# Kernel optimization log

Measured on AMD Instinct MI355X. Metric: run time of the kernel, lower is better.

## Reference

```python
import jax, jax.numpy as jnp
import numpy as np

S = 896.0          # image size in pixels
T = 28             # mask resolution
ALPHA, GAMMA = 0.25, 2.0
EPS = 1e-8
CAND_K = 10        # SimOTA candidate topk
CLS_W, L1_W, GIOU_W, MASK_W = 2.0, 5.0, 2.0, 5.0
CENTER_R = 0.05 * S  # center-region radius (approximates mmdet 2.5*stride)


def _areas(b):
    return jnp.clip(b[..., 2] - b[..., 0], 0) * jnp.clip(b[..., 3] - b[..., 1], 0)


def pairwise_iou_giou(a, b, eps=EPS):
    # a [n,4], b [m,4] xyxy -> (iou [n,m], giou [n,m])
    lt = jnp.maximum(a[:, None, :2], b[None, :, :2])
    rb = jnp.minimum(a[:, None, 2:], b[None, :, 2:])
    wh = jnp.clip(rb - lt, 0)
    inter = wh[..., 0] * wh[..., 1]
    union = _areas(a)[:, None] + _areas(b)[None, :] - inter
    iou = inter / (union + eps)
    elt = jnp.minimum(a[:, None, :2], b[None, :, :2])
    erb = jnp.maximum(a[:, None, 2:], b[None, :, 2:])
    ewh = jnp.clip(erb - elt, 0)
    enc = ewh[..., 0] * ewh[..., 1]
    return iou, iou - (enc - union) / (enc + eps)


def elementwise_giou(a, b, eps=EPS):
    # a,b [n,4] matched pairs -> giou [n] (the diag of generalized_box_iou)
    lt = jnp.maximum(a[:, :2], b[:, :2]); rb = jnp.minimum(a[:, 2:], b[:, 2:])
    wh = jnp.clip(rb - lt, 0); inter = wh[:, 0] * wh[:, 1]
    union = _areas(a) + _areas(b) - inter
    iou = inter / (union + eps)
    elt = jnp.minimum(a[:, :2], b[:, :2]); erb = jnp.maximum(a[:, 2:], b[:, 2:])
    ewh = jnp.clip(erb - elt, 0); enc = ewh[:, 0] * ewh[:, 1]
    return iou - (enc - union) / (enc + eps)


def crop_resize(img, box, scale, t=T):
    # img [C,H,W]; box [4] xyxy in image pixels; scale: pixels -> grid units.
    C, H, W = img.shape
    x1, y1, x2, y2 = box * scale
    xs = x1 + (x2 - x1) * (jnp.arange(t, dtype=img.dtype) + 0.5) / t - 0.5
    ys = y1 + (y2 - y1) * (jnp.arange(t, dtype=img.dtype) + 0.5) / t - 0.5
    X = jnp.broadcast_to(xs[None, :], (t, t))
    Y = jnp.broadcast_to(ys[:, None], (t, t))
    x0f = jnp.clip(jnp.floor(X), 0, W - 1); y0f = jnp.clip(jnp.floor(Y), 0, H - 1)
    wx = jnp.clip(X - x0f, 0, 1); wy = jnp.clip(Y - y0f, 0, 1)
    x0 = x0f.astype(jnp.int32); y0 = y0f.astype(jnp.int32)
    x1i = jnp.clip(x0 + 1, 0, W - 1); y1i = jnp.clip(y0 + 1, 0, H - 1)
    g = lambda yi, xi: img[:, yi, xi]  # [C,t,t]
    return (g(y0, x0) * (1 - wx) * (1 - wy) + g(y0, x1i) * wx * (1 - wy)
            + g(y1i, x0) * (1 - wx) * wy + g(y1i, x1i) * wx * wy)


def match_image(logits, boxes, gt_cls, gt_box):
    # SimOTA matcher (no-grad). logits [n,c], boxes [n,4] xyxy, gt_cls [m], gt_box [m,4]
    n, c = logits.shape
    m = gt_cls.shape[0]
    cx = (boxes[:, 0] + boxes[:, 2]) * 0.5
    cy = (boxes[:, 1] + boxes[:, 3]) * 0.5
    in_gt = ((cx[:, None] >= gt_box[None, :, 0]) & (cx[:, None] <= gt_box[None, :, 2])
             & (cy[:, None] >= gt_box[None, :, 1]) & (cy[:, None] <= gt_box[None, :, 3]))
    gcx = (gt_box[:, 0] + gt_box[:, 2]) * 0.5
    gcy = (gt_box[:, 1] + gt_box[:, 3]) * 0.5
    in_ct = ((jnp.abs(cx[:, None] - gcx[None, :]) <= CENTER_R)
             & (jnp.abs(cy[:, None] - gcy[None, :]) <= CENTER_R))
    valid = jnp.any(in_gt | in_ct, axis=1)              # [n]
    in_both = in_gt & in_ct                             # [n,m]
    # FocalLossCost (mmdet): pos - neg at gt class
    p = jax.nn.sigmoid(logits)
    neg = -jnp.log(1 - p + EPS) * (1 - ALPHA) * p ** GAMMA
    pos = -jnp.log(p + EPS) * ALPHA * (1 - p) ** GAMMA
    cls_cost = CLS_W * (pos - neg)[:, gt_cls]           # [n,m]
    nb = boxes / S; ngb = gt_box / S
    l1_cost = L1_W * jnp.sum(jnp.abs(nb[:, None, :] - ngb[None, :, :]), axis=-1)
    iou, _ = pairwise_iou_giou(boxes, gt_box)
    _, ngiou = pairwise_iou_giou(nb, ngb)
    cost = (cls_cost + l1_cost + GIOU_W * (1 - ngiou)
            + jnp.where(in_both, 0.0, 1e5) + jnp.where(valid[:, None], 0.0, 1e9))
    # dynamic-k assignment
    ious_v = jnp.where(valid[:, None], iou, 0.0)
    topk_ious, _ = jax.lax.top_k(ious_v.T, CAND_K)      # [m,CAND_K]
    dyn_k = jnp.clip(jnp.sum(topk_ious, axis=1).astype(jnp.int32), 1, n)
    ranks = jnp.argsort(jnp.argsort(cost, axis=0), axis=0)
    matching = (ranks < dyn_k[None, :]) & valid[:, None]
    best = jnp.argmin(cost, axis=1)
    multi = jnp.sum(matching, axis=1) > 1
    one_hot_best = jnp.arange(m)[None, :] == best[:, None]
    matching = jnp.where(multi[:, None], one_hot_best, matching)
    assigned = jnp.any(matching, axis=1)
    gt_ind = jnp.where(assigned, jnp.argmax(matching, axis=1), best)
    return valid, gt_ind


def image_loss(logits, boxes, feat, w_mask, gt_cls, gt_box, gt_mask):
    n, c = logits.shape
    sg = jax.lax.stop_gradient
    valid, gt_ind = match_image(sg(logits), sg(boxes), gt_cls, sg(gt_box))
    w = valid.astype(logits.dtype)
    mcls = gt_cls[gt_ind]                               # [n]
    mbox = gt_box[gt_ind]                               # [n,4]
    # sigmoid focal loss over all proposals; invalid ones get all-zero labels
    labels = (jnp.arange(c)[None, :] == mcls[:, None]).astype(logits.dtype) * w[:, None]
    p = jax.nn.sigmoid(logits)
    ce = jnp.logaddexp(0.0, logits) - logits * labels   # BCE-with-logits, stable
    p_t = p * labels + (1 - p) * (1 - labels)
    a_t = ALPHA * labels + (1 - ALPHA) * (1 - labels)
    cls_loss = jnp.sum(a_t * (1 - p_t) ** GAMMA * ce)
    nb = boxes / S; ngb = mbox / S
    l1_loss = jnp.sum(jnp.abs(nb - ngb) * w[:, None])
    giou_loss = jnp.sum((1 - elementwise_giou(nb, ngb)) * w)
    # mask head: ROI bilinear crop + per-class linear projection
    feat_scale = feat.shape[-1] / S
    crop = jax.vmap(lambda bx: crop_resize(feat, bx, feat_scale))(boxes)  # [n,Cf,T,T]
    wsel = w_mask[mcls]                                 # [n,Cf]
    m_pred = jax.nn.sigmoid(jnp.einsum('nfyx,nf->nyx', crop, wsel)).reshape(n, -1)
    mask_scale = gt_mask.shape[-1] / S
    gcrop = jax.vmap(lambda msk, bx: crop_resize(msk[None], bx, mask_scale)[0])(
        gt_mask[gt_ind], mbox).reshape(n, -1)
    inter = jnp.sum(m_pred * gcrop, axis=-1)
    union = jnp.sum(m_pred, axis=-1) + jnp.sum(gcrop, axis=-1) + EPS
    mask_loss = jnp.sum((1 - 2 * inter / union) * w)
    return cls_loss, l1_loss, giou_loss, mask_loss, jnp.sum(w)


def _make_boxes(key, shape, min_sz, max_sz):
    k1, k2 = jax.random.split(key)
    ctr = jax.random.uniform(k1, shape + (2,), minval=0.15 * S, maxval=0.85 * S)
    wh = jax.random.uniform(k2, shape + (2,), minval=min_sz, maxval=max_sz)
    return jnp.concatenate([jnp.clip(ctr - wh / 2, 0, S), jnp.clip(ctr + wh / 2, 0, S)], axis=-1)


def setup_inputs() -> dict:
    key = jax.random.key(0)
    ks = jax.random.split(key, 8)
    b, n, c, m, cf, hf, hm = 4, 300, 80, 24, 128, 64, 224
    return {
        'pred_logits': jax.random.normal(ks[0], (b, n, c), jnp.float32),
        'pred_boxes': _make_boxes(ks[1], (b, n), 20.0, 200.0),
        'features': jax.random.normal(ks[2], (b, cf, hf, hf), jnp.float32),
        'w_mask': jax.random.normal(ks[3], (c, cf), jnp.float32) * 0.05,
        'gt_classes': jax.random.randint(ks[4], (b, m), 0, c),
        'gt_boxes': _make_boxes(ks[5], (b, m), 80.0, 400.0),
        'gt_masks': (jax.random.uniform(ks[6], (b, m, hm, hm)) > 0.5).astype(jnp.float32),
    }


def reference(pred_logits, pred_boxes, features, w_mask, gt_classes, gt_boxes, gt_masks):
    per = jax.vmap(image_loss, in_axes=(0, 0, 0, None, 0, 0, 0))(
        pred_logits, pred_boxes, features, w_mask, gt_classes, gt_boxes, gt_masks)
    cls_l, l1_l, giou_l, mask_l, ninst = (jnp.sum(x) for x in per)
    # single diffusion stage (len(outputs) == 1)
    return jnp.stack([CLS_W * cls_l / ninst, L1_W * l1_l / ninst,
                      GIOU_W * giou_l / ninst, MASK_W * mask_l / ninst])
```

## Files before the change

### kernel.cpp

```cpp
#include <hip/hip_runtime.h>
#include <math.h>

#define N_PROP 300
#define N_CLS  80
#define N_GT   24
#define N_B    4
#define CF     128
#define HF     64
#define HM     224
#define TT     28
#define ALPHA  0.25f
#define EPSV   1e-8f
#define CAND_K 10
#define CENTER_R 44.8f
#define S_IMG 896.0f


__device__ __forceinline__ float iou_unnorm(const float* a, const float* g) {
    float lx = fmaxf(a[0], g[0]), ly = fmaxf(a[1], g[1]);
    float rx = fminf(a[2], g[2]), ry = fminf(a[3], g[3]);
    float w = fmaxf(rx - lx, 0.f), h = fmaxf(ry - ly, 0.f);
    float inter = w * h;
    float aa = fmaxf(a[2] - a[0], 0.f) * fmaxf(a[3] - a[1], 0.f);
    float ag = fmaxf(g[2] - g[0], 0.f) * fmaxf(g[3] - g[1], 0.f);
    float uni = aa + ag - inter;
    return inter / (uni + EPSV);
}

__device__ __forceinline__ float giou_pair(const float* a, const float* g) {
    float lx = fmaxf(a[0], g[0]), ly = fmaxf(a[1], g[1]);
    float rx = fminf(a[2], g[2]), ry = fminf(a[3], g[3]);
    float w = fmaxf(rx - lx, 0.f), h = fmaxf(ry - ly, 0.f);
    float inter = w * h;
    float aa = fmaxf(a[2] - a[0], 0.f) * fmaxf(a[3] - a[1], 0.f);
    float ag = fmaxf(g[2] - g[0], 0.f) * fmaxf(g[3] - g[1], 0.f);
    float uni = aa + ag - inter;
    float iou = inter / (uni + EPSV);
    float elx = fminf(a[0], g[0]), ely = fminf(a[1], g[1]);
    float erx = fmaxf(a[2], g[2]), ery = fmaxf(a[3], g[3]);
    float ew = fmaxf(erx - elx, 0.f), eh = fmaxf(ery - ely, 0.f);
    float enc = ew * eh;
    return iou - (enc - uni) / (enc + EPSV);
}

__device__ __forceinline__ float bilin(const float* img, int H, int W, float X, float Y) {
    float x0f = fminf(fmaxf(floorf(X), 0.f), (float)(W - 1));
    float y0f = fminf(fmaxf(floorf(Y), 0.f), (float)(H - 1));
    float wx = fminf(fmaxf(X - x0f, 0.f), 1.f);
    float wy = fminf(fmaxf(Y - y0f, 0.f), 1.f);
    int x0 = (int)x0f, y0 = (int)y0f;
    int x1 = min(x0 + 1, W - 1), y1 = min(y0 + 1, H - 1);
    float v00 = img[y0 * W + x0], v01 = img[y0 * W + x1];
    float v10 = img[y1 * W + x0], v11 = img[y1 * W + x1];
    return v00 * (1.f - wx) * (1.f - wy) + v01 * wx * (1.f - wy)
         + v10 * (1.f - wx) * wy + v11 * wx * wy;
}

__device__ __forceinline__ float focal_term(float x, float label) {
    float p = 1.f / (1.f + expf(-x));
    float ce = fmaxf(x, 0.f) + log1pf(expf(-fabsf(x))) - x * label;
    float pt = p * label + (1.f - p) * (1.f - label);
    float at = ALPHA * label + (1.f - ALPHA) * (1.f - label);
    return at * (1.f - pt) * (1.f - pt) * ce;
}

__global__ __launch_bounds__(256) void proj_kernel(
    const float* __restrict__ feat, const float* __restrict__ wm,
    const int* __restrict__ gtcls, float* __restrict__ proj)
{
    int blk = blockIdx.x;
    int b = blk >> 6;
    int chunk = blk & 63;
    int tid = threadIdx.x;

    __shared__ __align__(16) float s_w[CF][N_GT];
    __shared__ float s_acc[4][64][N_GT + 1];

    for (int k = tid; k < N_GT * CF; k += 256) {
        int j = k >> 7, f = k & 127;
        s_w[f][j] = wm[gtcls[b * N_GT + j] * CF + f];
    }
    __syncthreads();

    int px = tid & 63;
    int fq = tid >> 6;
    int pix = chunk * 64 + px;
    const float* fb = feat + ((size_t)b * CF + fq * 32) * (HF * HF) + pix;
    float accv[N_GT];
    #pragma unroll
    for (int j = 0; j < N_GT; j++) accv[j] = 0.f;
    #pragma unroll 8
    for (int f = 0; f < 32; f++) {
        float v = fb[(size_t)f * HF * HF];
        const float4* wrow = (const float4*)&s_w[fq * 32 + f][0];
        #pragma unroll
        for (int q = 0; q < 6; q++) {
            float4 wv = wrow[q];
            accv[q * 4 + 0] = fmaf(wv.x, v, accv[q * 4 + 0]);
            accv[q * 4 + 1] = fmaf(wv.y, v, accv[q * 4 + 1]);
            accv[q * 4 + 2] = fmaf(wv.z, v, accv[q * 4 + 2]);
            accv[q * 4 + 3] = fmaf(wv.w, v, accv[q * 4 + 3]);
        }
    }
    #pragma unroll
    for (int j = 0; j < N_GT; j++) s_acc[fq][px][j] = accv[j];
    __syncthreads();
    for (int o = tid; o < 64 * N_GT; o += 256) {
        int j = o >> 6, p2 = o & 63;
        float s = s_acc[0][p2][j] + s_acc[1][p2][j] + s_acc[2][p2][j] + s_acc[3][p2][j];
        proj[(size_t)(b * N_GT + j) * (HF * HF) + chunk * 64 + p2] = s;
    }
}

__global__ __launch_bounds__(320) void colmatch_kernel(
    const float* __restrict__ logits, const float* __restrict__ boxes,
    const int* __restrict__ gtcls, const float* __restrict__ gtbox,
    float* __restrict__ costT, unsigned int* __restrict__ matchcol)
{
    int bj = blockIdx.x;
    int b = bj / N_GT;
    int j = bj - b * N_GT;
    int tid = threadIdx.x;
    __shared__ float s_cost[N_PROP];
    __shared__ float s_iou[N_PROP];
    __shared__ float s_gball[N_GT][4];
    __shared__ int s_valid[N_PROP];
    __shared__ unsigned int s_match[10];

    if (tid < N_GT * 4) ((float*)s_gball)[tid] = gtbox[b * N_GT * 4 + tid];
    if (tid < 10) s_match[tid] = 0u;
    __syncthreads();

    int cls_j = gtcls[b * N_GT + j];
    if (tid < N_PROP) {
        int p = tid;
        const float* ap = boxes + (b * N_PROP + p) * 4;
        float a[4] = {ap[0], ap[1], ap[2], ap[3]};
        float cx = (a[0] + a[2]) * 0.5f;
        float cy = (a[1] + a[3]) * 0.5f;
        int any = 0, inb_j = 0;
        for (int q = 0; q < N_GT; q++) {
            const float* g = s_gball[q];
            int in_gt = (cx >= g[0]) & (cx <= g[2]) & (cy >= g[1]) & (cy <= g[3]);
            float gcx = (g[0] + g[2]) * 0.5f;
            float gcy = (g[1] + g[3]) * 0.5f;
            int in_ct = (fabsf(cx - gcx) <= CENTER_R) & (fabsf(cy - gcy) <= CENTER_R);
            any |= in_gt | in_ct;
            if (q == j) inb_j = in_gt & in_ct;
        }
        s_valid[p] = any;
        const float* g = s_gball[j];
        float x = logits[(size_t)(b * N_PROP + p) * N_CLS + cls_j];
        float pr = 1.f / (1.f + expf(-x));
        float neg = (-logf(1.f - pr + EPSV)) * (1.f - ALPHA) * (pr * pr);
        float pos = (-logf(pr + EPSV)) * ALPHA * ((1.f - pr) * (1.f - pr));
        float clsc = 2.0f * (pos - neg);
        float nb[4], ng[4];
        for (int k = 0; k < 4; k++) { nb[k] = a[k] / S_IMG; ng[k] = g[k] / S_IMG; }
        float l1 = 5.0f * (((fabsf(nb[0] - ng[0]) + fabsf(nb[1] - ng[1]))
                            + fabsf(nb[2] - ng[2])) + fabsf(nb[3] - ng[3]));
        float ngiou = giou_pair(nb, ng);
        float cst = clsc + l1;
        cst = cst + 2.0f * (1.f - ngiou);
        cst = cst + (inb_j ? 0.f : 1e5f);
        cst = cst + (any ? 0.f : 1e9f);
        s_cost[p] = cst;
        costT[(size_t)(b * N_PROP + p) * N_GT + j] = cst;
        s_iou[p] = any ? iou_unnorm(a, s_gball[j]) : 0.f;
    }
    __syncthreads();

    if (tid < 64) {
        int lane = tid;
        float iv[5]; int ii[5];
        #pragma unroll
        for (int c = 0; c < 5; c++) {
            int idx = c * 64 + lane;
            iv[c] = (idx < N_PROP) ? s_iou[idx] : -1.f;
            ii[c] = idx;
        }
        float ksum = 0.f;
        #pragma unroll
        for (int t = 0; t < CAND_K; t++) {
            float bv = iv[0]; int bi = ii[0];
            #pragma unroll
            for (int c = 1; c < 5; c++)
                if (iv[c] > bv || (iv[c] == bv && ii[c] < bi)) { bv = iv[c]; bi = ii[c]; }
            #pragma unroll
            for (int off = 1; off < 64; off <<= 1) {
                float ov = __shfl_xor(bv, off);
                int oi = __shfl_xor(bi, off);
                if (ov > bv || (ov == bv && oi < bi)) { bv = ov; bi = oi; }
            }
            ksum += bv;
            #pragma unroll
            for (int c = 0; c < 5; c++) if (ii[c] == bi) iv[c] = -1.f;
        }
        int dynk = max(1, min((int)ksum, N_PROP));

        float cv[5]; int ci[5];
        #pragma unroll
        for (int c = 0; c < 5; c++) {
            int idx = c * 64 + lane;
            cv[c] = (idx < N_PROP) ? s_cost[idx] : 3e38f;
            ci[c] = idx;
        }
        for (int t = 0; t < dynk; t++) {
            float bv = cv[0]; int bi = ci[0];
            #pragma unroll
            for (int c = 1; c < 5; c++)
                if (cv[c] < bv || (cv[c] == bv && ci[c] < bi)) { bv = cv[c]; bi = ci[c]; }
            #pragma unroll
            for (int off = 1; off < 64; off <<= 1) {
                float ov = __shfl_xor(bv, off);
                int oi = __shfl_xor(bi, off);
                if (ov < bv || (ov == bv && oi < bi)) { bv = ov; bi = oi; }
            }
            if (lane == 0 && s_valid[bi])
                s_match[bi >> 5] |= 1u << (bi & 31);
            #pragma unroll
            for (int c = 0; c < 5; c++) if (ci[c] == bi) cv[c] = 3e38f;
        }
    }
    __syncthreads();
    if (tid < 10) matchcol[bj * 10 + tid] = s_match[tid];
}

__global__ __launch_bounds__(256) void final_kernel(
    const float* __restrict__ logits, const float* __restrict__ boxes,
    const int* __restrict__ gtcls, const float* __restrict__ gtbox,
    const float* __restrict__ gmask, const float* __restrict__ costT,
    const unsigned int* __restrict__ matchcol, const float* __restrict__ proj,
    float* __restrict__ part)
{
    int e = blockIdx.x;
    int b = e / N_PROP;
    int i = e - b * N_PROP;
    int tid = threadIdx.x;

    __shared__ int s_gi, s_any;
    __shared__ float s_l1, s_gl;
    __shared__ float4 s_gbox;
    __shared__ float4 s_red[4];

    if (tid < 64) {
        int lane = tid;
        float4 a4 = ((const float4*)boxes)[e];
        int ql = (lane < N_GT) ? lane : 0;
        float4 g4 = ((const float4*)gtbox)[b * N_GT + ql];

        float cx = (a4.x + a4.z) * 0.5f;
        float cy = (a4.y + a4.w) * 0.5f;
        int vb = 0;
        if (lane < N_GT) {
            int in_gt = (cx >= g4.x) & (cx <= g4.z) & (cy >= g4.y) & (cy <= g4.w);
            float gcx = (g4.x + g4.z) * 0.5f;
            float gcy = (g4.y + g4.w) * 0.5f;
            int in_ct = (fabsf(cx - gcx) <= CENTER_R) & (fabsf(cy - gcy) <= CENTER_R);
            vb = in_gt | in_ct;
        }
        int any = (__ballot(vb) != 0ULL);
        float w = any ? 1.f : 0.f;

        float cv = 3e38f;
        int idx = 63;
        if (lane < N_GT) { cv = costT[(size_t)e * N_GT + lane]; idx = lane; }
        #pragma unroll
        for (int off = 1; off < 64; off <<= 1) {
            float oc = __shfl_xor(cv, off);
            int oi = __shfl_xor(idx, off);
            if (oc < cv || (oc == cv && oi < idx)) { cv = oc; idx = oi; }
        }
        int best = idx;

        int bit = 0;
        if (lane < N_GT)
            bit = (int)((matchcol[(b * N_GT + lane) * 10 + (i >> 5)] >> (i & 31)) & 1u);
        unsigned long long bm = __ballot(bit);
        int msk = (int)(bm & 0xFFFFFFULL);
        if (__popc(msk) > 1) msk = 1 << best;
        int gi = msk ? (__ffs(msk) - 1) : best;

        float gx = __shfl(g4.x, gi), gy = __shfl(g4.y, gi);
        float gz = __shfl(g4.z, gi), gw = __shfl(g4.w, gi);

        float l1 = 0.f, gl = 0.f;
        if (any) {
            float nb[4] = {a4.x / S_IMG, a4.y / S_IMG, a4.z / S_IMG, a4.w / S_IMG};
            float ng[4] = {gx / S_IMG, gy / S_IMG, gz / S_IMG, gw / S_IMG};
            l1 = (((fabsf(nb[0] - ng[0]) + fabsf(nb[1] - ng[1]))
                   + fabsf(nb[2] - ng[2])) + fabsf(nb[3] - ng[3]));
            gl = 1.f - giou_pair(nb, ng);
        }
        if (lane == 0) {
            s_gi = gi; s_any = any; s_l1 = l1; s_gl = gl;
            s_gbox = make_float4(gx, gy, gz, gw);
        }
    }
    __syncthreads();

    int gi = s_gi;
    int any = s_any;
    float w = any ? 1.f : 0.f;
    float4 a4 = ((const float4*)boxes)[e];
    float4 gb4 = s_gbox;

    int mc = gtcls[b * N_GT + gi];
    float clsv = 0.f;
    if (tid < N_CLS)
        clsv = focal_term(logits[(size_t)e * N_CLS + tid], (tid == mc) ? w : 0.f);

    float inter = 0.f, sp = 0.f, sg = 0.f;
    if (any) {
        const float* pimg = proj + (size_t)(b * N_GT + gi) * HF * HF;
        const float* gimg = gmask + (size_t)(b * N_GT + gi) * HM * HM;
        const float fs = 64.0f / 896.0f;
        const float ms = 224.0f / 896.0f;
        float px1 = a4.x * fs, py1 = a4.y * fs, px2 = a4.z * fs, py2 = a4.w * fs;
        float gx1 = gb4.x * ms, gy1 = gb4.y * ms, gx2 = gb4.z * ms, gy2 = gb4.w * ms;
        #pragma unroll 4
        for (int t = tid; t < TT * TT; t += 256) {
            int ty = t / TT, tx = t - ty * TT;
            float qx = ((float)tx + 0.5f) / (float)TT;
            float qy = ((float)ty + 0.5f) / (float)TT;
            float X = px1 + (px2 - px1) * qx - 0.5f;
            float Y = py1 + (py2 - py1) * qy - 0.5f;
            float lg = bilin(pimg, HF, HF, X, Y);
            float mp = 1.f / (1.f + expf(-lg));
            float Xg = gx1 + (gx2 - gx1) * qx - 0.5f;
            float Yg = gy1 + (gy2 - gy1) * qy - 0.5f;
            float gc = bilin(gimg, HM, HM, Xg, Yg);
            inter += mp * gc;
            sp += mp;
            sg += gc;
        }
    }

    #pragma unroll
    for (int off = 32; off > 0; off >>= 1) {
        clsv  += __shfl_xor(clsv, off);
        inter += __shfl_xor(inter, off);
        sp    += __shfl_xor(sp, off);
        sg    += __shfl_xor(sg, off);
    }
    if ((tid & 63) == 0) s_red[tid >> 6] = make_float4(clsv, inter, sp, sg);
    __syncthreads();
    if (tid == 0) {
        float4 t = s_red[0];
        for (int k = 1; k < 4; k++) {
            t.x += s_red[k].x; t.y += s_red[k].y; t.z += s_red[k].z; t.w += s_red[k].w;
        }
        float mterm = any ? (1.f - 2.f * t.y / (t.z + t.w + EPSV)) * w : 0.f;
        float* pp = part + (size_t)e * 8;
        *(float4*)pp = make_float4(t.x, any ? s_l1 : 0.f, any ? s_gl : 0.f, mterm);
        pp[4] = w;
    }
}

__global__ __launch_bounds__(256) void fin_kernel(
    const float* __restrict__ part, float* __restrict__ out)
{
    int tid = threadIdx.x;
    __shared__ float s_red[4][5];
    float s0 = 0.f, s1 = 0.f, s2 = 0.f, s3 = 0.f, s4 = 0.f;
    for (int p = tid; p < N_B * N_PROP; p += 256) {
        const float* pp = part + (size_t)p * 8;
        float4 v = *(const float4*)pp;
        s0 += v.x; s1 += v.y; s2 += v.z; s3 += v.w; s4 += pp[4];
    }
    #pragma unroll
    for (int off = 32; off > 0; off >>= 1) {
        s0 += __shfl_xor(s0, off);
        s1 += __shfl_xor(s1, off);
        s2 += __shfl_xor(s2, off);
        s3 += __shfl_xor(s3, off);
        s4 += __shfl_xor(s4, off);
    }
    if ((tid & 63) == 0) {
        int wv = tid >> 6;
        s_red[wv][0] = s0; s_red[wv][1] = s1; s_red[wv][2] = s2;
        s_red[wv][3] = s3; s_red[wv][4] = s4;
    }
    __syncthreads();
    if (tid == 0) {
        float t0 = 0.f, t1 = 0.f, t2 = 0.f, t3 = 0.f, t4 = 0.f;
        for (int k = 0; k < 4; k++) {
            t0 += s_red[k][0]; t1 += s_red[k][1]; t2 += s_red[k][2];
            t3 += s_red[k][3]; t4 += s_red[k][4];
        }
        out[0] = 2.0f * t0 / t4;
        out[1] = 5.0f * t1 / t4;
        out[2] = 2.0f * t2 / t4;
        out[3] = 5.0f * t3 / t4;
    }
}


extern "C" void kernel_launch(void* const* d_in, const int* in_sizes, int n_in,
                              void* d_out, int out_size, void* d_ws, size_t ws_size,
                              hipStream_t stream)
{
    const float* logits = (const float*)d_in[0];
    const float* boxes  = (const float*)d_in[1];
    const float* feat   = (const float*)d_in[2];
    const float* wm     = (const float*)d_in[3];
    const int*   gtcls  = (const int*)d_in[4];
    const float* gtbox  = (const float*)d_in[5];
    const float* gmask  = (const float*)d_in[6];
    float* out = (float*)d_out;
    float* ws  = (float*)d_ws;

    float* costT = ws;
    unsigned int* matchcol = (unsigned int*)(ws + 28800);
    float* part = ws + 28800 + 960;
    float* proj = ws + 28800 + 960 + 9600;

    hipLaunchKernelGGL(proj_kernel, dim3(N_B * 64), dim3(256), 0, stream,
                       feat, wm, gtcls, proj);
    hipLaunchKernelGGL(colmatch_kernel, dim3(N_B * N_GT), dim3(320), 0, stream,
                       logits, boxes, gtcls, gtbox, costT, matchcol);
    hipLaunchKernelGGL(final_kernel, dim3(N_B * N_PROP), dim3(256), 0, stream,
                       logits, boxes, gtcls, gtbox, gmask, costT, matchcol, proj, part);
    hipLaunchKernelGGL(fin_kernel, dim3(1), dim3(256), 0, stream, part, out);
}
```

Baseline: 116.1 us.

## Precompute GT mask crops once per GT and stage proj map in LDS

The resized 28x28 crop of each ground-truth mask, and its sum, depend only on the GT box and not on the proposal. They are now computed once per (image, GT) in extra blocks of the projection kernel and stored in workspace, so the final kernel no longer redoes the 224x224 bilinear gathers for every proposal. The final kernel also copies the matched 64x64 projected logit map and the GT crop into shared memory before sampling. The cost is a 16KB+ shared-memory copy per block, which may lower occupancy and adds a barrier.

```diff
diff --git a/kernel.cpp b/kernel.cpp
--- a/kernel.cpp
+++ b/kernel.cpp
@@ -64,51 +64,81 @@
     return at * (1.f - pt) * (1.f - pt) * ce;
 }
 
-__global__ __launch_bounds__(256) void proj_kernel(
+__global__ __launch_bounds__(256) void prep_kernel(
     const float* __restrict__ feat, const float* __restrict__ wm,
-    const int* __restrict__ gtcls, float* __restrict__ proj)
+    const int* __restrict__ gtcls, const float* __restrict__ gtbox,
+    const float* __restrict__ gmask, float* __restrict__ proj,
+    float* __restrict__ gcrop, float* __restrict__ gsum)
 {
     int blk = blockIdx.x;
-    int b = blk >> 6;
-    int chunk = blk & 63;
     int tid = threadIdx.x;
 
     __shared__ __align__(16) float s_w[CF][N_GT];
     __shared__ float s_acc[4][64][N_GT + 1];
-
-    for (int k = tid; k < N_GT * CF; k += 256) {
-        int j = k >> 7, f = k & 127;
-        s_w[f][j] = wm[gtcls[b * N_GT + j] * CF + f];
-    }
-    __syncthreads();
-
-    int px = tid & 63;
-    int fq = tid >> 6;
-    int pix = chunk * 64 + px;
-    const float* fb = feat + ((size_t)b * CF + fq * 32) * (HF * HF) + pix;
-    float accv[N_GT];
-    #pragma unroll
-    for (int j = 0; j < N_GT; j++) accv[j] = 0.f;
-    #pragma unroll 8
-    for (int f = 0; f < 32; f++) {
-        float v = fb[(size_t)f * HF * HF];
-        const float4* wrow = (const float4*)&s_w[fq * 32 + f][0];
-        #pragma unroll
-        for (int q = 0; q < 6; q++) {
-            float4 wv = wrow[q];
-            accv[q * 4 + 0] = fmaf(wv.x, v, accv[q * 4 + 0]);
-            accv[q * 4 + 1] = fmaf(wv.y, v, accv[q * 4 + 1]);
-            accv[q * 4 + 2] = fmaf(wv.z, v, accv[q * 4 + 2]);
-            accv[q * 4 + 3] = fmaf(wv.w, v, accv[q * 4 + 3]);
-        }
-    }
-    #pragma unroll
-    for (int j = 0; j < N_GT; j++) s_acc[fq][px][j] = accv[j];
-    __syncthreads();
-    for (int o = tid; o < 64 * N_GT; o += 256) {
-        int j = o >> 6, p2 = o & 63;
-        float s = s_acc[0][p2][j] + s_acc[1][p2][j] + s_acc[2][p2][j] + s_acc[3][p2][j];
-        proj[(size_t)(b * N_GT + j) * (HF * HF) + chunk * 64 + p2] = s;
+    __shared__ float s_rs[4];
+
+    if (blk < 256) {
+        int b = blk >> 6;
+        int chunk = blk & 63;
+        for (int k = tid; k < N_GT * CF; k += 256) {
+            int j = k >> 7, f = k & 127;
+            s_w[f][j] = wm[gtcls[b * N_GT + j] * CF + f];
+        }
+        __syncthreads();
+
+        int px = tid & 63;
+        int fq = tid >> 6;
+        int pix = chunk * 64 + px;
+        const float* fb = feat + ((size_t)b * CF + fq * 32) * (HF * HF) + pix;
+        float accv[N_GT];
+        #pragma unroll
+        for (int j = 0; j < N_GT; j++) accv[j] = 0.f;
+        #pragma unroll 8
+        for (int f = 0; f < 32; f++) {
+            float v = fb[(size_t)f * HF * HF];
+            const float4* wrow = (const float4*)&s_w[fq * 32 + f][0];
+            #pragma unroll
+            for (int q = 0; q < 6; q++) {
+                float4 wv = wrow[q];
+                accv[q * 4 + 0] = fmaf(wv.x, v, accv[q * 4 + 0]);
+                accv[q * 4 + 1] = fmaf(wv.y, v, accv[q * 4 + 1]);
+                accv[q * 4 + 2] = fmaf(wv.z, v, accv[q * 4 + 2]);
+                accv[q * 4 + 3] = fmaf(wv.w, v, accv[q * 4 + 3]);
+            }
+        }
+        #pragma unroll
+        for (int j = 0; j < N_GT; j++) s_acc[fq][px][j] = accv[j];
+        __syncthreads();
+        for (int o = tid; o < 64 * N_GT; o += 256) {
+            int j = o >> 6, p2 = o & 63;
+            float s = s_acc[0][p2][j] + s_acc[1][p2][j] + s_acc[2][p2][j] + s_acc[3][p2][j];
+            proj[(size_t)(b * N_GT + j) * (HF * HF) + chunk * 64 + p2] = s;
+        }
+    } else {
+        int bj = blk - 256;
+        int b = bj / N_GT;
+        int j = bj - b * N_GT;
+        const float* gimg = gmask + (size_t)(b * N_GT + j) * HM * HM;
+        float4 g4 = ((const float4*)gtbox)[b * N_GT + j];
+        const float ms = 224.0f / 896.0f;
+        float gx1 = g4.x * ms, gy1 = g4.y * ms, gx2 = g4.z * ms, gy2 = g4.w * ms;
+        float sg = 0.f;
+        #pragma unroll 4
+        for (int t = tid; t < TT * TT; t += 256) {
+            int ty = t / TT, tx = t - ty * TT;
+            float qx = ((float)tx + 0.5f) / (float)TT;
+            float qy = ((float)ty + 0.5f) / (float)TT;
+            float Xg = gx1 + (gx2 - gx1) * qx - 0.5f;
+            float Yg = gy1 + (gy2 - gy1) * qy - 0.5f;
+            float gc = bilin(gimg, HM, HM, Xg, Yg);
+            gcrop[(size_t)bj * (TT * TT) + t] = gc;
+            sg += gc;
+        }
+        #pragma unroll
+        for (int off = 32; off > 0; off >>= 1) sg += __shfl_xor(sg, off);
+        if ((tid & 63) == 0) s_rs[tid >> 6] = sg;
+        __syncthreads();
+        if (tid == 0) gsum[bj] = ((s_rs[0] + s_rs[1]) + s_rs[2]) + s_rs[3];
     }
 }
 
@@ -229,9 +259,9 @@
 __global__ __launch_bounds__(256) void final_kernel(
     const float* __restrict__ logits, const float* __restrict__ boxes,
     const int* __restrict__ gtcls, const float* __restrict__ gtbox,
-    const float* __restrict__ gmask, const float* __restrict__ costT,
-    const unsigned int* __restrict__ matchcol, const float* __restrict__ proj,
-    float* __restrict__ part)
+    const float* __restrict__ costT, const unsigned int* __restrict__ matchcol,
+    const float* __restrict__ proj, const float* __restrict__ gcrop,
+    const float* __restrict__ gsum, float* __restrict__ part)
 {
     int e = blockIdx.x;
     int b = e / N_PROP;
@@ -240,8 +270,9 @@
 
     __shared__ int s_gi, s_any;
     __shared__ float s_l1, s_gl;
-    __shared__ float4 s_gbox;
     __shared__ float4 s_red[4];
+    __shared__ float s_pmap[HF * HF];
+    __shared__ float s_gc[TT * TT];
 
     if (tid < 64) {
         int lane = tid;
@@ -294,7 +325,6 @@
         }
         if (lane == 0) {
             s_gi = gi; s_any = any; s_l1 = l1; s_gl = gl;
-            s_gbox = make_float4(gx, gy, gz, gw);
         }
     }
     __syncthreads();
@@ -302,22 +332,25 @@
     int gi = s_gi;
     int any = s_any;
     float w = any ? 1.f : 0.f;
-    float4 a4 = ((const float4*)boxes)[e];
-    float4 gb4 = s_gbox;
+
+    if (any) {
+        const float* pimg = proj + (size_t)(b * N_GT + gi) * (HF * HF);
+        const float* gcr = gcrop + (size_t)(b * N_GT + gi) * (TT * TT);
+        for (int k = tid; k < HF * HF; k += 256) s_pmap[k] = pimg[k];
+        for (int k = tid; k < TT * TT; k += 256) s_gc[k] = gcr[k];
+    }
 
     int mc = gtcls[b * N_GT + gi];
     float clsv = 0.f;
     if (tid < N_CLS)
         clsv = focal_term(logits[(size_t)e * N_CLS + tid], (tid == mc) ? w : 0.f);
-
-    float inter = 0.f, sp = 0.f, sg = 0.f;
+    __syncthreads();
+
+    float inter = 0.f, sp = 0.f;
     if (any) {
-        const float* pimg = proj + (size_t)(b * N_GT + gi) * HF * HF;
-        const float* gimg = gmask + (size_t)(b * N_GT + gi) * HM * HM;
+        float4 a4 = ((const float4*)boxes)[e];
         const float fs = 64.0f / 896.0f;
-        const float ms = 224.0f / 896.0f;
         float px1 = a4.x * fs, py1 = a4.y * fs, px2 = a4.z * fs, py2 = a4.w * fs;
-        float gx1 = gb4.x * ms, gy1 = gb4.y * ms, gx2 = gb4.z * ms, gy2 = gb4.w * ms;
         #pragma unroll 4
         for (int t = tid; t < TT * TT; t += 256) {
             int ty = t / TT, tx = t - ty * TT;
@@ -325,14 +358,10 @@
             float qy = ((float)ty + 0.5f) / (float)TT;
             float X = px1 + (px2 - px1) * qx - 0.5f;
             float Y = py1 + (py2 - py1) * qy - 0.5f;
-            float lg = bilin(pimg, HF, HF, X, Y);
+            float lg = bilin(s_pmap, HF, HF, X, Y);
             float mp = 1.f / (1.f + expf(-lg));
-            float Xg = gx1 + (gx2 - gx1) * qx - 0.5f;
-            float Yg = gy1 + (gy2 - gy1) * qy - 0.5f;
-            float gc = bilin(gimg, HM, HM, Xg, Yg);
-            inter += mp * gc;
+            inter += mp * s_gc[t];
             sp += mp;
-            sg += gc;
         }
     }
 
@@ -341,16 +370,16 @@
         clsv  += __shfl_xor(clsv, off);
         inter += __shfl_xor(inter, off);
         sp    += __shfl_xor(sp, off);
-        sg    += __shfl_xor(sg, off);
-    }
-    if ((tid & 63) == 0) s_red[tid >> 6] = make_float4(clsv, inter, sp, sg);
+    }
+    if ((tid & 63) == 0) s_red[tid >> 6] = make_float4(clsv, inter, sp, 0.f);
     __syncthreads();
     if (tid == 0) {
         float4 t = s_red[0];
         for (int k = 1; k < 4; k++) {
-            t.x += s_red[k].x; t.y += s_red[k].y; t.z += s_red[k].z; t.w += s_red[k].w;
-        }
-        float mterm = any ? (1.f - 2.f * t.y / (t.z + t.w + EPSV)) * w : 0.f;
+            t.x += s_red[k].x; t.y += s_red[k].y; t.z += s_red[k].z;
+        }
+        float sg = any ? gsum[b * N_GT + gi] : 0.f;
+        float mterm = any ? (1.f - 2.f * t.y / (t.z + sg + EPSV)) * w : 0.f;
         float* pp = part + (size_t)e * 8;
         *(float4*)pp = make_float4(t.x, any ? s_l1 : 0.f, any ? s_gl : 0.f, mterm);
         pp[4] = w;
@@ -412,14 +441,16 @@
 
     float* costT = ws;
     unsigned int* matchcol = (unsigned int*)(ws + 28800);
-    float* part = ws + 28800 + 960;
-    float* proj = ws + 28800 + 960 + 9600;
-
-    hipLaunchKernelGGL(proj_kernel, dim3(N_B * 64), dim3(256), 0, stream,
-                       feat, wm, gtcls, proj);
+    float* part  = ws + 28800 + 960;
+    float* proj  = ws + 28800 + 960 + 9600;
+    float* gcrop = proj + 393216;
+    float* gsum  = gcrop + 75264;
+
+    hipLaunchKernelGGL(prep_kernel, dim3(256 + N_B * N_GT), dim3(256), 0, stream,
+                       feat, wm, gtcls, gtbox, gmask, proj, gcrop, gsum);
     hipLaunchKernelGGL(colmatch_kernel, dim3(N_B * N_GT), dim3(320), 0, stream,
                        logits, boxes, gtcls, gtbox, costT, matchcol);
     hipLaunchKernelGGL(final_kernel, dim3(N_B * N_PROP), dim3(256), 0, stream,
-                       logits, boxes, gtcls, gtbox, gmask, costT, matchcol, proj, part);
+                       logits, boxes, gtcls, gtbox, costT, matchcol, proj, gcrop, gsum, part);
     hipLaunchKernelGGL(fin_kernel, dim3(1), dim3(256), 0, stream, part, out);
 }
```

Result: no change. 117.4 us (+1.2%).
